# Performance work log

Hardware: AMD Instinct MI355X
Metric: run time of the kernel (lower is better)

The kernel has to match this reference:

```python
import jax, jax.numpy as jnp
import numpy as np

K3 = 27            # kernel_size**3
PAIRS_PER_K = 131072  # pairs per kernel offset (equal-size segments)
N_VOX = 262144     # active voxels (stride-1, same grid: N_in == N_out)
C_IN = 32
C_OUT = 32


def setup_inputs() -> dict:
    key = jax.random.key(0)
    k1, k2, k3, k4 = jax.random.split(key, 4)
    M = K3 * PAIRS_PER_K
    in_feature = jax.random.normal(k1, (N_VOX, C_IN), dtype=jnp.float32)
    kernel = jax.random.normal(k2, (K3, C_IN, C_OUT), dtype=jnp.float32) * (1.0 / np.sqrt(C_IN * K3))
    bias = jax.random.normal(k3, (C_OUT,), dtype=jnp.float32) * 0.01
    # nbmap[:, 0] = input voxel index, nbmap[:, 1] = output voxel index,
    # sorted by kernel offset (offset k owns rows [k*P, (k+1)*P)).
    nbmap = jax.random.randint(k4, (M, 2), 0, N_VOX, dtype=jnp.int32)
    nbsizes = jnp.full((K3,), PAIRS_PER_K, dtype=jnp.int32)
    return {"in_feature": in_feature, "kernel": kernel, "bias": bias,
            "nbmap": nbmap, "nbsizes": nbsizes}


def reference(in_feature, kernel, bias, nbmap, nbsizes):
    """Gather -> per-offset GEMM -> scatter-add, matching
    ext.conv.sparse_convolution for a stride-1 non-transposed conv where
    nbmap rows are grouped by kernel offset with equal segment sizes."""
    k3, c_in, c_out = kernel.shape
    m = nbmap.shape[0]
    p = m // k3  # pairs per offset (static)
    n_out = in_feature.shape[0]  # same grid, stride 1
    # gather input features for every (input, output) pair  [M, C_in]
    gathered = in_feature[nbmap[:, 0]]
    # batched GEMM: one [P, C_in] x [C_in, C_out] per kernel offset
    contrib = jnp.einsum('kpi,kio->kpo', gathered.reshape(k3, p, c_in), kernel)
    contrib = contrib.reshape(m, c_out)
    # scatter-add contributions into output voxels
    out = jax.ops.segment_sum(contrib, nbmap[:, 1], num_segments=n_out)
    return out + bias
```

## Files before the change

### kernel.cpp

```cpp
#include <hip/hip_runtime.h>
#include <hip/hip_bf16.h>


#define N_VOX    262144
#define LOG2_NV  18
#define C_CH     32
#define K3       27
#define LOG2_PPK 17
#define BLOCK    256
#define FLAG_FIN 0x40000000
#define ECAP     4096
#define PLPAD    36
#define FRAGN    (K3 * 2 * 64)
#define NF16     (N_VOX * 4)

typedef __attribute__((ext_vector_type(8))) short bf16x8;
typedef __attribute__((ext_vector_type(4))) float f32x4;

__device__ __forceinline__ unsigned short f2bf(float f) {
  union { __hip_bfloat16 h; unsigned short u; } cv;
  cv.h = __float2bfloat16(f);
  return cv.u;
}

__global__ __launch_bounds__(BLOCK) void setup_kernel(
    int4* __restrict__ clrT, long nt4, int4* __restrict__ clrC, long nc4,
    const float* __restrict__ in_feature, unsigned short* __restrict__ feat16,
    int use16, const float* __restrict__ kernel_w,
    unsigned short* __restrict__ Bf) {
  long idx = (long)blockIdx.x * BLOCK + threadIdx.x;
  if (idx < nt4) {
    clrT[idx] = make_int4(-1, -1, -1, -1);
    return;
  }
  idx -= nt4;
  if (idx < nc4) {
    clrC[idx] = make_int4(0, 0, 0, 0);
    return;
  }
  idx -= nc4;
  if (use16) {
    if (idx < NF16) {
      const float4* src = (const float4*)in_feature + (idx << 1);
      float4 f0 = src[0], f1 = src[1];
      union { unsigned short u[8]; uint4 v; } pk;
      pk.u[0] = f2bf(f0.x); pk.u[1] = f2bf(f0.y);
      pk.u[2] = f2bf(f0.z); pk.u[3] = f2bf(f0.w);
      pk.u[4] = f2bf(f1.x); pk.u[5] = f2bf(f1.y);
      pk.u[6] = f2bf(f1.z); pk.u[7] = f2bf(f1.w);
      ((uint4*)feat16)[idx] = pk.v;
      return;
    }
    idx -= NF16;
  }
  if (idx < FRAGN) {
    int wid = (int)idx;
    int lane = wid & 63;
    int kc = wid >> 6;
    int k = kc >> 1, t = kc & 1;
    int i0 = (lane >> 4) * 8;
    int c = t * 16 + (lane & 15);
    union { unsigned short u[8]; uint4 v; } pk;
#pragma unroll
    for (int j = 0; j < 8; ++j)
      pk.u[j] = f2bf(kernel_w[(k << 10) + (i0 + j) * C_CH + c]);
    ((uint4*)Bf)[wid] = pk.v;
  }
}

__global__ __launch_bounds__(BLOCK) void passA_kernel(
    const int4* __restrict__ nbmap2, int* __restrict__ T, int Mq) {
  int q = blockIdx.x * BLOCK + threadIdx.x;
  if (q >= Mq) return;
  int4 na = nbmap2[q * 2];
  int4 nb = nbmap2[q * 2 + 1];
  int p0 = q << 2, p1 = p0 | 1, p2 = p0 | 2, p3 = p0 | 3;
  T[((p0 >> LOG2_PPK) << LOG2_NV) + na.y] = p0;
  T[((p1 >> LOG2_PPK) << LOG2_NV) + na.w] = p1;
  T[((p2 >> LOG2_PPK) << LOG2_NV) + nb.y] = p2;
  T[((p3 >> LOG2_PPK) << LOG2_NV) + nb.w] = p3;
}

__device__ __forceinline__ void loser_path(
    int vox, int k, int in, int* __restrict__ T2, int idx, int use2,
    int* __restrict__ ovf_cnt, int* __restrict__ ovf, int S2,
    int* __restrict__ ecnt, int2* __restrict__ elist) {
  int val = in;
  if (use2) {
    val = atomicExch(&T2[idx], val);
    if (val < 0) return;
  }
  int pos = atomicAdd(&ovf_cnt[vox], 1);
  if (pos < S2) {
    ovf[(pos << LOG2_NV) + vox] = (k << LOG2_NV) | val;
  } else {
    int ep = atomicAdd(ecnt, 1);
    if (ep < ECAP) elist[ep] = make_int2(vox, (k << LOG2_NV) | val);
  }
}

__global__ __launch_bounds__(BLOCK) void passB_kernel(
    const int4* __restrict__ nbmap2, int* __restrict__ T, int* __restrict__ T2,
    int use2, int* __restrict__ ovf_cnt, int* __restrict__ ovf, int S2,
    int* __restrict__ ecnt, int2* __restrict__ elist, int Mq) {
  int q = blockIdx.x * BLOCK + threadIdx.x;
  if (q >= Mq) return;
  int4 na = nbmap2[q * 2];
  int4 nb = nbmap2[q * 2 + 1];
  int p0 = q << 2, p1 = p0 | 1, p2 = p0 | 2, p3 = p0 | 3;
  int idx0 = ((p0 >> LOG2_PPK) << LOG2_NV) + na.y;
  int idx1 = ((p1 >> LOG2_PPK) << LOG2_NV) + na.w;
  int idx2 = ((p2 >> LOG2_PPK) << LOG2_NV) + nb.y;
  int idx3 = ((p3 >> LOG2_PPK) << LOG2_NV) + nb.w;
  int t0 = T[idx0];
  int t1 = T[idx1];
  int t2 = T[idx2];
  int t3 = T[idx3];
  if (t0 == p0) T[idx0] = FLAG_FIN | na.x;
  else loser_path(na.y, p0 >> LOG2_PPK, na.x, T2, idx0, use2, ovf_cnt, ovf,
                  S2, ecnt, elist);
  if (t1 == p1) T[idx1] = FLAG_FIN | na.z;
  else loser_path(na.w, p1 >> LOG2_PPK, na.z, T2, idx1, use2, ovf_cnt, ovf,
                  S2, ecnt, elist);
  if (t2 == p2) T[idx2] = FLAG_FIN | nb.x;
  else loser_path(nb.y, p2 >> LOG2_PPK, nb.x, T2, idx2, use2, ovf_cnt, ovf,
                  S2, ecnt, elist);
  if (t3 == p3) T[idx3] = FLAG_FIN | nb.z;
  else loser_path(nb.w, p3 >> LOG2_PPK, nb.z, T2, idx3, use2, ovf_cnt, ovf,
                  S2, ecnt, elist);
}

template <int F16>
__global__ __launch_bounds__(BLOCK, 4) void gather_splitk_kernel(
    const float* __restrict__ in_feature,
    const unsigned short* __restrict__ feat16,
    const float* __restrict__ kernel_w,
    const float* __restrict__ bias,
    const int* __restrict__ T,
    const int* __restrict__ T2, int use2,
    const int* __restrict__ ovf_cnt,
    const int* __restrict__ ovf,
    const unsigned short* __restrict__ Bf,
    float* __restrict__ out, int S2) {
  __shared__ float plane[4][16][PLPAD];
  __shared__ int flatE[256];
  __shared__ int scnt[16];

  const int tid = threadIdx.x;
  const int w = tid >> 6;
  const int lane = tid & 63;
  const int r16 = lane & 15;
  const int quad = lane >> 4;
  const int vb = blockIdx.x << 4;

  const int er = tid & 15;
  const int ej = tid >> 4;
  int eval = 0;
  if (ej < S2)
    eval = ovf[(ej << LOG2_NV) + vb + er];
  if (tid < 16) {
    int c = ovf_cnt[vb + tid];
    scnt[tid] = c < S2 ? c : S2;
  }
  const int kb = w * 7;
  const int kn = (w == 3) ? 6 : 7;
  const int v = vb + r16;
  int tv[7];
#pragma unroll
  for (int d = 0; d < 7; ++d)
    tv[d] = (d < kn) ? T[((kb + d) << LOG2_NV) + v] : -1;
  __syncthreads();

  int myb = 0, tot = 0;
#pragma unroll
  for (int q = 0; q < 16; ++q) {
    int cq = scnt[q];
    if (q < er) myb += cq;
    tot += cq;
  }
  if (ej < scnt[er])
    flatE[myb + ej] = (er << 24) | eval;
  __syncthreads();

  int tv2[7];
#pragma unroll
  for (int d = 0; d < 7; ++d)
    tv2[d] = (use2 && d < kn) ? T2[((kb + d) << LOG2_NV) + v] : -1;

  bf16x8 R0[7], R1[7];
#pragma unroll
  for (int d = 0; d < 7; ++d) {
    int t = tv[d];
    int in = (t >= 0) ? (t & 0x3FFFF) : 0;
    bf16x8 a;
    if (F16) {
      a = *reinterpret_cast<const bf16x8*>(feat16 + (in << 5) + (quad << 3));
    } else {
      const float4* ap = (const float4*)(in_feature + (in << 5) + (quad << 3));
      float4 f0 = ap[0], f1 = ap[1];
      a[0] = (short)f2bf(f0.x); a[1] = (short)f2bf(f0.y);
      a[2] = (short)f2bf(f0.z); a[3] = (short)f2bf(f0.w);
      a[4] = (short)f2bf(f1.x); a[5] = (short)f2bf(f1.y);
      a[6] = (short)f2bf(f1.z); a[7] = (short)f2bf(f1.w);
    }
    if (t < 0) a = (bf16x8)0;
    R0[d] = a;
  }
#pragma unroll
  for (int d = 0; d < 7; ++d) {
    int t = tv2[d];
    int in = (t >= 0) ? (t & 0x3FFFF) : 0;
    bf16x8 a;
    if (F16) {
      a = *reinterpret_cast<const bf16x8*>(feat16 + (in << 5) + (quad << 3));
    } else {
      const float4* ap = (const float4*)(in_feature + (in << 5) + (quad << 3));
      float4 f0 = ap[0], f1 = ap[1];
      a[0] = (short)f2bf(f0.x); a[1] = (short)f2bf(f0.y);
      a[2] = (short)f2bf(f0.z); a[3] = (short)f2bf(f0.w);
      a[4] = (short)f2bf(f1.x); a[5] = (short)f2bf(f1.y);
      a[6] = (short)f2bf(f1.z); a[7] = (short)f2bf(f1.w);
    }
    if (t < 0) a = (bf16x8)0;
    R1[d] = a;
  }

  f32x4 acc0 = {0.f, 0.f, 0.f, 0.f};
  f32x4 acc1 = {0.f, 0.f, 0.f, 0.f};
  const uint4* bfp = (const uint4*)Bf;
#pragma unroll
  for (int d = 0; d < 7; ++d) {
    if (d < kn) {
      int k = kb + d;
      uint4 h0 = bfp[(k * 2 + 0) * 64 + lane];
      uint4 h1 = bfp[(k * 2 + 1) * 64 + lane];
      acc0 = __builtin_amdgcn_mfma_f32_16x16x32_bf16(
          R0[d], *reinterpret_cast<const bf16x8*>(&h0), acc0, 0, 0, 0);
      acc1 = __builtin_amdgcn_mfma_f32_16x16x32_bf16(
          R0[d], *reinterpret_cast<const bf16x8*>(&h1), acc1, 0, 0, 0);
    }
  }
  if (use2) {
#pragma unroll
    for (int d = 0; d < 7; ++d) {
      if (d < kn) {
        int k = kb + d;
        uint4 h0 = bfp[(k * 2 + 0) * 64 + lane];
        uint4 h1 = bfp[(k * 2 + 1) * 64 + lane];
        acc0 = __builtin_amdgcn_mfma_f32_16x16x32_bf16(
            R1[d], *reinterpret_cast<const bf16x8*>(&h0), acc0, 0, 0, 0);
        acc1 = __builtin_amdgcn_mfma_f32_16x16x32_bf16(
            R1[d], *reinterpret_cast<const bf16x8*>(&h1), acc1, 0, 0, 0);
      }
    }
  }

#pragma unroll
  for (int reg = 0; reg < 4; ++reg) {
    int row = quad * 4 + reg;
    plane[w][row][r16] = acc0[reg];
    plane[w][row][16 + r16] = acc1[reg];
  }

  const int c32 = lane & 31, h = lane >> 5;
  int i = w;
  int e_cur = 0;
  float4 p0, p1, p2, p3;
  if (i < tot) {
    e_cur = flatE[i];
    const float4* ar =
        (const float4*)(in_feature + ((e_cur & 0x3FFFF) << 5) + (h << 4));
    p0 = ar[0]; p1 = ar[1]; p2 = ar[2]; p3 = ar[3];
  }
  while (i < tot) {
    const int e = e_cur;
    float4 q0 = p0, q1 = p1, q2 = p2, q3 = p3;
    const int inext = i + 4;
    if (inext < tot) {
      e_cur = flatE[inext];
      const float4* ar =
          (const float4*)(in_feature + ((e_cur & 0x3FFFF) << 5) + (h << 4));
      p0 = ar[0]; p1 = ar[1]; p2 = ar[2]; p3 = ar[3];
    }
    const int k2 = (e >> LOG2_NV) & 31;
    const int rr = (e >> 24) & 15;
    const float* wcol = kernel_w + (k2 << 10) + (h << 4) * C_CH + c32;
    float psum = 0.f;
    psum = fmaf(q0.x, wcol[0 * C_CH], psum);
    psum = fmaf(q0.y, wcol[1 * C_CH], psum);
    psum = fmaf(q0.z, wcol[2 * C_CH], psum);
    psum = fmaf(q0.w, wcol[3 * C_CH], psum);
    psum = fmaf(q1.x, wcol[4 * C_CH], psum);
    psum = fmaf(q1.y, wcol[5 * C_CH], psum);
    psum = fmaf(q1.z, wcol[6 * C_CH], psum);
    psum = fmaf(q1.w, wcol[7 * C_CH], psum);
    psum = fmaf(q2.x, wcol[8 * C_CH], psum);
    psum = fmaf(q2.y, wcol[9 * C_CH], psum);
    psum = fmaf(q2.z, wcol[10 * C_CH], psum);
    psum = fmaf(q2.w, wcol[11 * C_CH], psum);
    psum = fmaf(q3.x, wcol[12 * C_CH], psum);
    psum = fmaf(q3.y, wcol[13 * C_CH], psum);
    psum = fmaf(q3.z, wcol[14 * C_CH], psum);
    psum = fmaf(q3.w, wcol[15 * C_CH], psum);
    psum += __shfl_xor(psum, 32);
    if (h == 0) plane[w][rr][c32] += psum;
    i = inext;
  }

  __syncthreads();
  const int mr = tid >> 4;
  const int mc = (tid & 15) << 1;
  float s0 = plane[0][mr][mc] + plane[1][mr][mc] + plane[2][mr][mc] +
             plane[3][mr][mc] + bias[mc];
  float s1 = plane[0][mr][mc + 1] + plane[1][mr][mc + 1] +
             plane[2][mr][mc + 1] + plane[3][mr][mc + 1] + bias[mc + 1];
  float2 o; o.x = s0; o.y = s1;
  *(float2*)(out + ((vb + mr) << 5) + mc) = o;
}

__global__ __launch_bounds__(BLOCK) void emergency_kernel(
    const float* __restrict__ in_feature, const float* __restrict__ kernel_w,
    const int* __restrict__ ecnt, const int2* __restrict__ elist,
    float* __restrict__ out) {
  int e = blockIdx.x * BLOCK + threadIdx.x;
  int n = *ecnt;
  if (n > ECAP) n = ECAP;
  if (e >= n) return;
  int2 ent = elist[e];
  int v = ent.x, k = ent.y >> LOG2_NV, in = ent.y & 0x3FFFF;
  float a[C_CH];
  const float4* ar = (const float4*)(in_feature + (in << 5));
#pragma unroll
  for (int q = 0; q < 8; ++q) ((float4*)a)[q] = ar[q];
  for (int c = 0; c < C_CH; ++c) {
    float s = 0.f;
#pragma unroll
    for (int i = 0; i < C_CH; ++i)
      s = fmaf(a[i], kernel_w[(k << 10) + i * C_CH + c], s);
    atomicAdd(&out[v * C_CH + c], s);
  }
}

__global__ __launch_bounds__(BLOCK) void init_bias_kernel(
    float* __restrict__ out, const float* __restrict__ bias, int n4) {
  int idx = blockIdx.x * blockDim.x + threadIdx.x;
  if (idx >= n4) return;
  ((float4*)out)[idx] = ((const float4*)bias)[idx & 7];
}

__global__ __launch_bounds__(BLOCK) void scatter_conv_kernel(
    const float* __restrict__ in_feature, const float* __restrict__ kernel_w,
    const int* __restrict__ nbmap, float* __restrict__ out) {
  const int k = blockIdx.x >> 9;
  const int pair = blockIdx.x * BLOCK + threadIdx.x;
  const float* __restrict__ Wk = kernel_w + k * (C_CH * C_CH);
  const int2 nb = ((const int2*)nbmap)[pair];
  const float4* __restrict__ inrow =
      (const float4*)(in_feature + (long)nb.x * C_CH);
  float a[C_CH];
#pragma unroll
  for (int j = 0; j < 8; ++j) ((float4*)a)[j] = inrow[j];
  float acc[C_CH];
#pragma unroll
  for (int c = 0; c < C_CH; ++c) acc[c] = 0.0f;
#pragma unroll
  for (int i = 0; i < C_CH; ++i) {
    const float av = a[i];
#pragma unroll
    for (int c = 0; c < C_CH; ++c)
      acc[c] = fmaf(av, Wk[i * C_CH + c], acc[c]);
  }
  float* __restrict__ orow = out + (long)nb.y * C_CH;
#pragma unroll
  for (int c = 0; c < C_CH; ++c) atomicAdd(orow + c, acc[c]);
}

extern "C" void kernel_launch(void* const* d_in, const int* in_sizes, int n_in,
                              void* d_out, int out_size, void* d_ws,
                              size_t ws_size, hipStream_t stream) {
  const float* in_feature = (const float*)d_in[0];
  const float* kernel_w   = (const float*)d_in[1];
  const float* bias       = (const float*)d_in[2];
  const int*   nbmap      = (const int*)d_in[3];
  float* out = (float*)d_out;
  const int M = in_sizes[3] / 2;
  const int Mq = M / 4;

  const long FIXED = 64 + 2 * ECAP + 13824;
  long ws_ints = (long)(ws_size / 4);
  long planes = (ws_ints - FIXED) / N_VOX;
  int use2 = 0, use16 = 0;
  long s2c;
  if (planes >= 75) {
    use2 = 1; use16 = 1;
    s2c = planes - 71;
    if (s2c > 7) s2c = 7;
  } else if (planes >= 59) {
    use2 = 1;
    s2c = planes - 55;
    if (s2c > 7) s2c = 7;
  } else {
    s2c = planes - 28;
    if (s2c > 15) s2c = 15;
  }
  int S2 = (int)s2c;

  if (!use2 && S2 < 4) {
    const int n4 = out_size / 4;
    init_bias_kernel<<<(n4 + BLOCK - 1) / BLOCK, BLOCK, 0, stream>>>(out, bias,
                                                                     n4);
    scatter_conv_kernel<<<M / BLOCK, BLOCK, 0, stream>>>(in_feature, kernel_w,
                                                         nbmap, out);
    return;
  }

  const long TPLANES = (long)K3 * N_VOX;
  int* T        = (int*)d_ws;
  int* T2       = use2 ? (T + TPLANES) : T;
  int* ovf_cnt  = T + TPLANES * (1 + use2);
  int* ecnt     = ovf_cnt + N_VOX;
  int2* elist   = (int2*)(ecnt + 64);
  unsigned short* Bf = (unsigned short*)(ecnt + 64 + 2 * ECAP);
  int* ovf      = ((int*)Bf) + 13824;
  unsigned short* feat16 = (unsigned short*)(ovf + (long)S2 * N_VOX);

  const long nt4 = TPLANES * (1 + use2) / 4;
  const long nc4 = (N_VOX + 64) / 4;
  const long total = nt4 + nc4 + (use16 ? (long)NF16 : 0) + FRAGN;
  const long sblocks = (total + BLOCK - 1) / BLOCK;
  setup_kernel<<<(int)sblocks, BLOCK, 0, stream>>>(
      (int4*)T, nt4, (int4*)ovf_cnt, nc4, in_feature, feat16, use16, kernel_w,
      Bf);

  passA_kernel<<<(Mq + BLOCK - 1) / BLOCK, BLOCK, 0, stream>>>(
      (const int4*)nbmap, T, Mq);
  passB_kernel<<<(Mq + BLOCK - 1) / BLOCK, BLOCK, 0, stream>>>(
      (const int4*)nbmap, T, T2, use2, ovf_cnt, ovf, S2, ecnt, elist, Mq);
  if (use16)
    gather_splitk_kernel<1><<<N_VOX / 16, BLOCK, 0, stream>>>(
        in_feature, feat16, kernel_w, bias, T, T2, use2, ovf_cnt, ovf, Bf,
        out, S2);
  else
    gather_splitk_kernel<0><<<N_VOX / 16, BLOCK, 0, stream>>>(
        in_feature, feat16, kernel_w, bias, T, T2, use2, ovf_cnt, ovf, Bf,
        out, S2);
  emergency_kernel<<<ECAP / BLOCK, BLOCK, 0, stream>>>(in_feature, kernel_w,
                                                       ecnt, elist, out);
}
```

Measured before the change: 393.9 us.

## Pack primary and secondary slot into one 64-bit table entry per (offset, voxel)

Replaces the two separate 32-bit tables T and T2 with a single 64-bit table whose entries hold the winning pair id, its input index, and a second input index. Pass A writes pair id and input together, so pass B no longer needs to write winners back, and losers claim the second slot with a 64-bit CAS instead of an atomicExch on a separate plane. The gather kernel then reads one 8-byte word per offset instead of two scattered 4-byte reads. The aim is fewer random memory transactions in passes B and gather, at the cost of CAS retry loops and wider stores in pass A.

```diff
diff --git a/kernel.cpp b/kernel.cpp
--- a/kernel.cpp
+++ b/kernel.cpp
@@ -16,6 +16,10 @@
 
 typedef __attribute__((ext_vector_type(8))) short bf16x8;
 typedef __attribute__((ext_vector_type(4))) float f32x4;
+typedef unsigned long long ull;
+
+#define PMASK   0x3FFFFFull
+#define EMPTY2(w) (((w) >> 58) == 0x3Full)
 
 __device__ __forceinline__ unsigned short f2bf(float f) {
   union { __hip_bfloat16 h; unsigned short u; } cv;
@@ -68,76 +72,105 @@
   }
 }
 
-__global__ __launch_bounds__(BLOCK) void passA_kernel(
-    const int4* __restrict__ nbmap2, int* __restrict__ T, int Mq) {
+__global__ __launch_bounds__(BLOCK) void passA_packed(
+    const int4* __restrict__ nbmap2, ull* __restrict__ T64, int Mq) {
   int q = blockIdx.x * BLOCK + threadIdx.x;
   if (q >= Mq) return;
   int4 na = nbmap2[q * 2];
   int4 nb = nbmap2[q * 2 + 1];
   int p0 = q << 2, p1 = p0 | 1, p2 = p0 | 2, p3 = p0 | 3;
-  T[((p0 >> LOG2_PPK) << LOG2_NV) + na.y] = p0;
-  T[((p1 >> LOG2_PPK) << LOG2_NV) + na.w] = p1;
-  T[((p2 >> LOG2_PPK) << LOG2_NV) + nb.y] = p2;
-  T[((p3 >> LOG2_PPK) << LOG2_NV) + nb.w] = p3;
-}
-
-__device__ __forceinline__ void loser_path(
-    int vox, int k, int in, int* __restrict__ T2, int idx, int use2,
+  const ull EM = 0x3Full << 58;
+  T64[((long)(p0 >> LOG2_PPK) << LOG2_NV) + na.y] =
+      (ull)p0 | ((ull)na.x << 22) | EM;
+  T64[((long)(p1 >> LOG2_PPK) << LOG2_NV) + na.w] =
+      (ull)p1 | ((ull)na.z << 22) | EM;
+  T64[((long)(p2 >> LOG2_PPK) << LOG2_NV) + nb.y] =
+      (ull)p2 | ((ull)nb.x << 22) | EM;
+  T64[((long)(p3 >> LOG2_PPK) << LOG2_NV) + nb.w] =
+      (ull)p3 | ((ull)nb.z << 22) | EM;
+}
+
+__device__ __forceinline__ void ovf_push(
+    int vox, int k, int in, int* __restrict__ ovf_cnt, int* __restrict__ ovf,
+    int S2, int* __restrict__ ecnt, int2* __restrict__ elist) {
+  int pos = atomicAdd(&ovf_cnt[vox], 1);
+  if (pos < S2) {
+    ovf[(pos << LOG2_NV) + vox] = (k << LOG2_NV) | in;
+  } else {
+    int ep = atomicAdd(ecnt, 1);
+    if (ep < ECAP) elist[ep] = make_int2(vox, (k << LOG2_NV) | in);
+  }
+}
+
+__device__ __forceinline__ void resolve_packed(
+    int p, int vox, int in, ull w, ull* __restrict__ T64, long idx,
     int* __restrict__ ovf_cnt, int* __restrict__ ovf, int S2,
     int* __restrict__ ecnt, int2* __restrict__ elist) {
-  int val = in;
-  if (use2) {
-    val = atomicExch(&T2[idx], val);
-    if (val < 0) return;
-  }
-  int pos = atomicAdd(&ovf_cnt[vox], 1);
-  if (pos < S2) {
-    ovf[(pos << LOG2_NV) + vox] = (k << LOG2_NV) | val;
-  } else {
-    int ep = atomicAdd(ecnt, 1);
-    if (ep < ECAP) elist[ep] = make_int2(vox, (k << LOG2_NV) | val);
-  }
-}
-
-__global__ __launch_bounds__(BLOCK) void passB_kernel(
-    const int4* __restrict__ nbmap2, int* __restrict__ T, int* __restrict__ T2,
-    int use2, int* __restrict__ ovf_cnt, int* __restrict__ ovf, int S2,
+  if ((w & PMASK) == (ull)p) return;
+  ull cur = w;
+  for (;;) {
+    if (!EMPTY2(cur)) break;
+    ull nw = (cur & ((1ull << 40) - 1)) | ((ull)in << 40);
+    ull old = atomicCAS(&T64[idx], cur, nw);
+    if (old == cur) return;
+    cur = old;
+  }
+  ovf_push(vox, p >> LOG2_PPK, in, ovf_cnt, ovf, S2, ecnt, elist);
+}
+
+__global__ __launch_bounds__(BLOCK) void passB_packed(
+    const int4* __restrict__ nbmap2, ull* __restrict__ T64,
+    int* __restrict__ ovf_cnt, int* __restrict__ ovf, int S2,
     int* __restrict__ ecnt, int2* __restrict__ elist, int Mq) {
   int q = blockIdx.x * BLOCK + threadIdx.x;
   if (q >= Mq) return;
   int4 na = nbmap2[q * 2];
   int4 nb = nbmap2[q * 2 + 1];
   int p0 = q << 2, p1 = p0 | 1, p2 = p0 | 2, p3 = p0 | 3;
-  int idx0 = ((p0 >> LOG2_PPK) << LOG2_NV) + na.y;
-  int idx1 = ((p1 >> LOG2_PPK) << LOG2_NV) + na.w;
-  int idx2 = ((p2 >> LOG2_PPK) << LOG2_NV) + nb.y;
-  int idx3 = ((p3 >> LOG2_PPK) << LOG2_NV) + nb.w;
-  int t0 = T[idx0];
-  int t1 = T[idx1];
-  int t2 = T[idx2];
-  int t3 = T[idx3];
-  if (t0 == p0) T[idx0] = FLAG_FIN | na.x;
-  else loser_path(na.y, p0 >> LOG2_PPK, na.x, T2, idx0, use2, ovf_cnt, ovf,
-                  S2, ecnt, elist);
-  if (t1 == p1) T[idx1] = FLAG_FIN | na.z;
-  else loser_path(na.w, p1 >> LOG2_PPK, na.z, T2, idx1, use2, ovf_cnt, ovf,
-                  S2, ecnt, elist);
-  if (t2 == p2) T[idx2] = FLAG_FIN | nb.x;
-  else loser_path(nb.y, p2 >> LOG2_PPK, nb.x, T2, idx2, use2, ovf_cnt, ovf,
-                  S2, ecnt, elist);
-  if (t3 == p3) T[idx3] = FLAG_FIN | nb.z;
-  else loser_path(nb.w, p3 >> LOG2_PPK, nb.z, T2, idx3, use2, ovf_cnt, ovf,
-                  S2, ecnt, elist);
-}
-
-template <int F16>
+  long i0 = ((long)(p0 >> LOG2_PPK) << LOG2_NV) + na.y;
+  long i1 = ((long)(p1 >> LOG2_PPK) << LOG2_NV) + na.w;
+  long i2 = ((long)(p2 >> LOG2_PPK) << LOG2_NV) + nb.y;
+  long i3 = ((long)(p3 >> LOG2_PPK) << LOG2_NV) + nb.w;
+  ull w0 = T64[i0];
+  ull w1 = T64[i1];
+  ull w2 = T64[i2];
+  ull w3 = T64[i3];
+  resolve_packed(p0, na.y, na.x, w0, T64, i0, ovf_cnt, ovf, S2, ecnt, elist);
+  resolve_packed(p1, na.w, na.z, w1, T64, i1, ovf_cnt, ovf, S2, ecnt, elist);
+  resolve_packed(p2, nb.y, nb.x, w2, T64, i2, ovf_cnt, ovf, S2, ecnt, elist);
+  resolve_packed(p3, nb.w, nb.z, w3, T64, i3, ovf_cnt, ovf, S2, ecnt, elist);
+}
+
+__global__ __launch_bounds__(BLOCK) void passA_legacy(
+    const int2* __restrict__ nbmap, int* __restrict__ T, int M) {
+  int p = blockIdx.x * BLOCK + threadIdx.x;
+  if (p >= M) return;
+  int2 nb = nbmap[p];
+  T[((p >> LOG2_PPK) << LOG2_NV) + nb.y] = p;
+}
+
+__global__ __launch_bounds__(BLOCK) void passB_legacy(
+    const int2* __restrict__ nbmap, int* __restrict__ T,
+    int* __restrict__ ovf_cnt, int* __restrict__ ovf, int S2,
+    int* __restrict__ ecnt, int2* __restrict__ elist, int M) {
+  int p = blockIdx.x * BLOCK + threadIdx.x;
+  if (p >= M) return;
+  int2 nb = nbmap[p];
+  int idx = ((p >> LOG2_PPK) << LOG2_NV) + nb.y;
+  if (T[idx] == p) {
+    T[idx] = FLAG_FIN | nb.x;
+  } else {
+    ovf_push(nb.y, p >> LOG2_PPK, nb.x, ovf_cnt, ovf, S2, ecnt, elist);
+  }
+}
+
+template <int PACKED, int F16>
 __global__ __launch_bounds__(BLOCK, 4) void gather_splitk_kernel(
     const float* __restrict__ in_feature,
     const unsigned short* __restrict__ feat16,
     const float* __restrict__ kernel_w,
     const float* __restrict__ bias,
-    const int* __restrict__ T,
-    const int* __restrict__ T2, int use2,
+    const void* __restrict__ Tv,
     const int* __restrict__ ovf_cnt,
     const int* __restrict__ ovf,
     const unsigned short* __restrict__ Bf,
@@ -165,10 +198,22 @@
   const int kb = w * 7;
   const int kn = (w == 3) ? 6 : 7;
   const int v = vb + r16;
-  int tv[7];
-#pragma unroll
-  for (int d = 0; d < 7; ++d)
-    tv[d] = (d < kn) ? T[((kb + d) << LOG2_NV) + v] : -1;
+
+  ull wv[7];
+  if (PACKED) {
+    const ull* T64 = (const ull*)Tv;
+#pragma unroll
+    for (int d = 0; d < 7; ++d)
+      wv[d] = (d < kn) ? T64[((long)(kb + d) << LOG2_NV) + v] : ~0ull;
+  } else {
+    const int* T = (const int*)Tv;
+#pragma unroll
+    for (int d = 0; d < 7; ++d) {
+      int t = (d < kn) ? T[((kb + d) << LOG2_NV) + v] : -1;
+      wv[d] = (t >= 0) ? (((ull)(t & 0x3FFFF) << 22) | (0x3Full << 58))
+                       : ~0ull;
+    }
+  }
   __syncthreads();
 
   int myb = 0, tot = 0;
@@ -182,16 +227,11 @@
     flatE[myb + ej] = (er << 24) | eval;
   __syncthreads();
 
-  int tv2[7];
-#pragma unroll
-  for (int d = 0; d < 7; ++d)
-    tv2[d] = (use2 && d < kn) ? T2[((kb + d) << LOG2_NV) + v] : -1;
-
   bf16x8 R0[7], R1[7];
 #pragma unroll
   for (int d = 0; d < 7; ++d) {
-    int t = tv[d];
-    int in = (t >= 0) ? (t & 0x3FFFF) : 0;
+    bool val1 = (wv[d] & PMASK) != PMASK;
+    int in = val1 ? (int)((wv[d] >> 22) & 0x3FFFF) : 0;
     bf16x8 a;
     if (F16) {
       a = *reinterpret_cast<const bf16x8*>(feat16 + (in << 5) + (quad << 3));
@@ -203,26 +243,29 @@
       a[4] = (short)f2bf(f1.x); a[5] = (short)f2bf(f1.y);
       a[6] = (short)f2bf(f1.z); a[7] = (short)f2bf(f1.w);
     }
-    if (t < 0) a = (bf16x8)0;
+    if (!val1) a = (bf16x8)0;
     R0[d] = a;
   }
-#pragma unroll
-  for (int d = 0; d < 7; ++d) {
-    int t = tv2[d];
-    int in = (t >= 0) ? (t & 0x3FFFF) : 0;
-    bf16x8 a;
-    if (F16) {
-      a = *reinterpret_cast<const bf16x8*>(feat16 + (in << 5) + (quad << 3));
-    } else {
-      const float4* ap = (const float4*)(in_feature + (in << 5) + (quad << 3));
-      float4 f0 = ap[0], f1 = ap[1];
-      a[0] = (short)f2bf(f0.x); a[1] = (short)f2bf(f0.y);
-      a[2] = (short)f2bf(f0.z); a[3] = (short)f2bf(f0.w);
-      a[4] = (short)f2bf(f1.x); a[5] = (short)f2bf(f1.y);
-      a[6] = (short)f2bf(f1.z); a[7] = (short)f2bf(f1.w);
-    }
-    if (t < 0) a = (bf16x8)0;
-    R1[d] = a;
+  if (PACKED) {
+#pragma unroll
+    for (int d = 0; d < 7; ++d) {
+      bool val2 = !EMPTY2(wv[d]);
+      int in = val2 ? (int)((wv[d] >> 40) & 0x3FFFF) : 0;
+      bf16x8 a;
+      if (F16) {
+        a = *reinterpret_cast<const bf16x8*>(feat16 + (in << 5) + (quad << 3));
+      } else {
+        const float4* ap =
+            (const float4*)(in_feature + (in << 5) + (quad << 3));
+        float4 f0 = ap[0], f1 = ap[1];
+        a[0] = (short)f2bf(f0.x); a[1] = (short)f2bf(f0.y);
+        a[2] = (short)f2bf(f0.z); a[3] = (short)f2bf(f0.w);
+        a[4] = (short)f2bf(f1.x); a[5] = (short)f2bf(f1.y);
+        a[6] = (short)f2bf(f1.z); a[7] = (short)f2bf(f1.w);
+      }
+      if (!val2) a = (bf16x8)0;
+      R1[d] = a;
+    }
   }
 
   f32x4 acc0 = {0.f, 0.f, 0.f, 0.f};
@@ -240,7 +283,7 @@
           R0[d], *reinterpret_cast<const bf16x8*>(&h1), acc1, 0, 0, 0);
     }
   }
-  if (use2) {
+  if (PACKED) {
 #pragma unroll
     for (int d = 0; d < 7; ++d) {
       if (d < kn) {
@@ -389,14 +432,14 @@
   const long FIXED = 64 + 2 * ECAP + 13824;
   long ws_ints = (long)(ws_size / 4);
   long planes = (ws_ints - FIXED) / N_VOX;
-  int use2 = 0, use16 = 0;
+  int packed = 0, use16 = 0;
   long s2c;
   if (planes >= 75) {
-    use2 = 1; use16 = 1;
+    packed = 1; use16 = 1;
     s2c = planes - 71;
     if (s2c > 7) s2c = 7;
   } else if (planes >= 59) {
-    use2 = 1;
+    packed = 1;
     s2c = planes - 55;
     if (s2c > 7) s2c = 7;
   } else {
@@ -405,7 +448,7 @@
   }
   int S2 = (int)s2c;
 
-  if (!use2 && S2 < 4) {
+  if (!packed && S2 < 4) {
     const int n4 = out_size / 4;
     init_bias_kernel<<<(n4 + BLOCK - 1) / BLOCK, BLOCK, 0, stream>>>(out, bias,
                                                                      n4);
@@ -414,36 +457,45 @@
     return;
   }
 
-  const long TPLANES = (long)K3 * N_VOX;
-  int* T        = (int*)d_ws;
-  int* T2       = use2 ? (T + TPLANES) : T;
-  int* ovf_cnt  = T + TPLANES * (1 + use2);
+  const long planesT = packed ? 2L * K3 : (long)K3;
+  int* Tbase    = (int*)d_ws;
+  int* ovf_cnt  = Tbase + planesT * N_VOX;
   int* ecnt     = ovf_cnt + N_VOX;
   int2* elist   = (int2*)(ecnt + 64);
   unsigned short* Bf = (unsigned short*)(ecnt + 64 + 2 * ECAP);
   int* ovf      = ((int*)Bf) + 13824;
   unsigned short* feat16 = (unsigned short*)(ovf + (long)S2 * N_VOX);
 
-  const long nt4 = TPLANES * (1 + use2) / 4;
+  const long nt4 = planesT * N_VOX / 4;
   const long nc4 = (N_VOX + 64) / 4;
   const long total = nt4 + nc4 + (use16 ? (long)NF16 : 0) + FRAGN;
   const long sblocks = (total + BLOCK - 1) / BLOCK;
   setup_kernel<<<(int)sblocks, BLOCK, 0, stream>>>(
-      (int4*)T, nt4, (int4*)ovf_cnt, nc4, in_feature, feat16, use16, kernel_w,
-      Bf);
-
-  passA_kernel<<<(Mq + BLOCK - 1) / BLOCK, BLOCK, 0, stream>>>(
-      (const int4*)nbmap, T, Mq);
-  passB_kernel<<<(Mq + BLOCK - 1) / BLOCK, BLOCK, 0, stream>>>(
-      (const int4*)nbmap, T, T2, use2, ovf_cnt, ovf, S2, ecnt, elist, Mq);
-  if (use16)
-    gather_splitk_kernel<1><<<N_VOX / 16, BLOCK, 0, stream>>>(
-        in_feature, feat16, kernel_w, bias, T, T2, use2, ovf_cnt, ovf, Bf,
-        out, S2);
-  else
-    gather_splitk_kernel<0><<<N_VOX / 16, BLOCK, 0, stream>>>(
-        in_feature, feat16, kernel_w, bias, T, T2, use2, ovf_cnt, ovf, Bf,
-        out, S2);
+      (int4*)Tbase, nt4, (int4*)ovf_cnt, nc4, in_feature, feat16, use16,
+      kernel_w, Bf);
+
+  if (packed) {
+    passA_packed<<<(Mq + BLOCK - 1) / BLOCK, BLOCK, 0, stream>>>(
+        (const int4*)nbmap, (ull*)Tbase, Mq);
+    passB_packed<<<(Mq + BLOCK - 1) / BLOCK, BLOCK, 0, stream>>>(
+        (const int4*)nbmap, (ull*)Tbase, ovf_cnt, ovf, S2, ecnt, elist, Mq);
+    if (use16)
+      gather_splitk_kernel<1, 1><<<N_VOX / 16, BLOCK, 0, stream>>>(
+          in_feature, feat16, kernel_w, bias, (const void*)Tbase, ovf_cnt,
+          ovf, Bf, out, S2);
+    else
+      gather_splitk_kernel<1, 0><<<N_VOX / 16, BLOCK, 0, stream>>>(
+          in_feature, feat16, kernel_w, bias, (const void*)Tbase, ovf_cnt,
+          ovf, Bf, out, S2);
+  } else {
+    passA_legacy<<<(M + BLOCK - 1) / BLOCK, BLOCK, 0, stream>>>(
+        (const int2*)nbmap, Tbase, M);
+    passB_legacy<<<(M + BLOCK - 1) / BLOCK, BLOCK, 0, stream>>>(
+        (const int2*)nbmap, Tbase, ovf_cnt, ovf, S2, ecnt, elist, M);
+    gather_splitk_kernel<0, 0><<<N_VOX / 16, BLOCK, 0, stream>>>(
+        in_feature, feat16, kernel_w, bias, (const void*)Tbase, ovf_cnt, ovf,
+        Bf, out, S2);
+  }
   emergency_kernel<<<ECAP / BLOCK, BLOCK, 0, stream>>>(in_feature, kernel_w,
                                                        ecnt, elist, out);
 }
```

After: 362.0 us, median of 3. -8.1%, faster.

## Replace dense per-offset tables with sliced bucketed pair lists for gather

Applied to the files above, without the earlier changes.

Drops the two dense K3×N_VOX lookup planes and the two-pass claim/overflow scheme. A single scatter pass appends each pair into per-16-voxel buckets, split into 8 slices to spread atomic contention. The gather kernel now builds the per-offset slots in shared memory from those buckets, and the emergency list is folded into the gather kernel, so the separate fallback kernel launch is gone. This removes clearing and reading ~56 MB of tables, at the cost of global atomics on bucket counters, LDS atomics, and every block scanning the global overflow list.

```diff
diff --git a/kernel.cpp b/kernel.cpp
--- a/kernel.cpp
+++ b/kernel.cpp
@@ -8,11 +8,13 @@
 #define K3       27
 #define LOG2_PPK 17
 #define BLOCK    256
-#define FLAG_FIN 0x40000000
 #define ECAP     4096
 #define PLPAD    36
 #define FRAGN    (K3 * 2 * 64)
 #define NF16     (N_VOX * 4)
+#define NBUCK    16384
+#define SCAP     64
+#define NSLOT    (K3 * 16)
 
 typedef __attribute__((ext_vector_type(8))) short bf16x8;
 typedef __attribute__((ext_vector_type(4))) float f32x4;
@@ -24,16 +26,11 @@
 }
 
 __global__ __launch_bounds__(BLOCK) void setup_kernel(
-    int4* __restrict__ clrT, long nt4, int4* __restrict__ clrC, long nc4,
+    int4* __restrict__ clrC, long nc4,
     const float* __restrict__ in_feature, unsigned short* __restrict__ feat16,
     int use16, const float* __restrict__ kernel_w,
     unsigned short* __restrict__ Bf) {
   long idx = (long)blockIdx.x * BLOCK + threadIdx.x;
-  if (idx < nt4) {
-    clrT[idx] = make_int4(-1, -1, -1, -1);
-    return;
-  }
-  idx -= nt4;
   if (idx < nc4) {
     clrC[idx] = make_int4(0, 0, 0, 0);
     return;
@@ -68,130 +65,112 @@
   }
 }
 
-__global__ __launch_bounds__(BLOCK) void passA_kernel(
-    const int4* __restrict__ nbmap2, int* __restrict__ T, int Mq) {
+__device__ __forceinline__ void put_pair(
+    int vox, int in, int k, int slice, int* __restrict__ cnt,
+    int* __restrict__ bucket, int* __restrict__ ecnt,
+    int2* __restrict__ elist) {
+  int sb = slice * NBUCK + (vox >> 4);
+  int pos = atomicAdd(&cnt[sb], 1);
+  if (pos < SCAP) {
+    bucket[(long)sb * SCAP + pos] = (k << 22) | ((vox & 15) << 18) | in;
+  } else {
+    int ep = atomicAdd(ecnt, 1);
+    if (ep < ECAP) elist[ep] = make_int2(vox, (k << LOG2_NV) | in);
+  }
+}
+
+__global__ __launch_bounds__(BLOCK) void scatter_pairs(
+    const int4* __restrict__ nbmap2, int* __restrict__ cnt,
+    int* __restrict__ bucket, int* __restrict__ ecnt,
+    int2* __restrict__ elist, int Mq) {
   int q = blockIdx.x * BLOCK + threadIdx.x;
   if (q >= Mq) return;
+  int slice = blockIdx.x & 7;
   int4 na = nbmap2[q * 2];
   int4 nb = nbmap2[q * 2 + 1];
-  int p0 = q << 2, p1 = p0 | 1, p2 = p0 | 2, p3 = p0 | 3;
-  T[((p0 >> LOG2_PPK) << LOG2_NV) + na.y] = p0;
-  T[((p1 >> LOG2_PPK) << LOG2_NV) + na.w] = p1;
-  T[((p2 >> LOG2_PPK) << LOG2_NV) + nb.y] = p2;
-  T[((p3 >> LOG2_PPK) << LOG2_NV) + nb.w] = p3;
-}
-
-__device__ __forceinline__ void loser_path(
-    int vox, int k, int in, int* __restrict__ T2, int idx, int use2,
-    int* __restrict__ ovf_cnt, int* __restrict__ ovf, int S2,
-    int* __restrict__ ecnt, int2* __restrict__ elist) {
-  int val = in;
-  if (use2) {
-    val = atomicExch(&T2[idx], val);
-    if (val < 0) return;
-  }
-  int pos = atomicAdd(&ovf_cnt[vox], 1);
-  if (pos < S2) {
-    ovf[(pos << LOG2_NV) + vox] = (k << LOG2_NV) | val;
-  } else {
-    int ep = atomicAdd(ecnt, 1);
-    if (ep < ECAP) elist[ep] = make_int2(vox, (k << LOG2_NV) | val);
-  }
-}
-
-__global__ __launch_bounds__(BLOCK) void passB_kernel(
-    const int4* __restrict__ nbmap2, int* __restrict__ T, int* __restrict__ T2,
-    int use2, int* __restrict__ ovf_cnt, int* __restrict__ ovf, int S2,
-    int* __restrict__ ecnt, int2* __restrict__ elist, int Mq) {
-  int q = blockIdx.x * BLOCK + threadIdx.x;
-  if (q >= Mq) return;
-  int4 na = nbmap2[q * 2];
-  int4 nb = nbmap2[q * 2 + 1];
-  int p0 = q << 2, p1 = p0 | 1, p2 = p0 | 2, p3 = p0 | 3;
-  int idx0 = ((p0 >> LOG2_PPK) << LOG2_NV) + na.y;
-  int idx1 = ((p1 >> LOG2_PPK) << LOG2_NV) + na.w;
-  int idx2 = ((p2 >> LOG2_PPK) << LOG2_NV) + nb.y;
-  int idx3 = ((p3 >> LOG2_PPK) << LOG2_NV) + nb.w;
-  int t0 = T[idx0];
-  int t1 = T[idx1];
-  int t2 = T[idx2];
-  int t3 = T[idx3];
-  if (t0 == p0) T[idx0] = FLAG_FIN | na.x;
-  else loser_path(na.y, p0 >> LOG2_PPK, na.x, T2, idx0, use2, ovf_cnt, ovf,
-                  S2, ecnt, elist);
-  if (t1 == p1) T[idx1] = FLAG_FIN | na.z;
-  else loser_path(na.w, p1 >> LOG2_PPK, na.z, T2, idx1, use2, ovf_cnt, ovf,
-                  S2, ecnt, elist);
-  if (t2 == p2) T[idx2] = FLAG_FIN | nb.x;
-  else loser_path(nb.y, p2 >> LOG2_PPK, nb.x, T2, idx2, use2, ovf_cnt, ovf,
-                  S2, ecnt, elist);
-  if (t3 == p3) T[idx3] = FLAG_FIN | nb.z;
-  else loser_path(nb.w, p3 >> LOG2_PPK, nb.z, T2, idx3, use2, ovf_cnt, ovf,
-                  S2, ecnt, elist);
+  int p0 = q << 2;
+  put_pair(na.y, na.x, (p0 | 0) >> LOG2_PPK, slice, cnt, bucket, ecnt, elist);
+  put_pair(na.w, na.z, (p0 | 1) >> LOG2_PPK, slice, cnt, bucket, ecnt, elist);
+  put_pair(nb.y, nb.x, (p0 | 2) >> LOG2_PPK, slice, cnt, bucket, ecnt, elist);
+  put_pair(nb.w, nb.z, (p0 | 3) >> LOG2_PPK, slice, cnt, bucket, ecnt, elist);
 }
 
 template <int F16>
-__global__ __launch_bounds__(BLOCK, 4) void gather_splitk_kernel(
+__global__ __launch_bounds__(BLOCK, 4) void gather_csr_kernel(
     const float* __restrict__ in_feature,
     const unsigned short* __restrict__ feat16,
     const float* __restrict__ kernel_w,
     const float* __restrict__ bias,
-    const int* __restrict__ T,
-    const int* __restrict__ T2, int use2,
-    const int* __restrict__ ovf_cnt,
-    const int* __restrict__ ovf,
+    const int* __restrict__ cnt,
+    const int* __restrict__ bucket,
+    const int* __restrict__ ecnt,
+    const int2* __restrict__ elist,
     const unsigned short* __restrict__ Bf,
-    float* __restrict__ out, int S2) {
+    float* __restrict__ out) {
   __shared__ float plane[4][16][PLPAD];
-  __shared__ int flatE[256];
-  __shared__ int scnt[16];
+  __shared__ int flatE[320];
+  __shared__ int ls1[NSLOT], ls2[NSLOT];
+  __shared__ int lcnt[NSLOT];
+  __shared__ int scn[8];
+  __shared__ int extraN;
 
   const int tid = threadIdx.x;
   const int w = tid >> 6;
   const int lane = tid & 63;
   const int r16 = lane & 15;
   const int quad = lane >> 4;
-  const int vb = blockIdx.x << 4;
-
-  const int er = tid & 15;
-  const int ej = tid >> 4;
-  int eval = 0;
-  if (ej < S2)
-    eval = ovf[(ej << LOG2_NV) + vb + er];
-  if (tid < 16) {
-    int c = ovf_cnt[vb + tid];
-    scnt[tid] = c < S2 ? c : S2;
-  }
+  const int b = blockIdx.x;
+  const int vb = b << 4;
+
+  for (int i = tid; i < NSLOT; i += BLOCK) {
+    ls1[i] = -1; ls2[i] = -1; lcnt[i] = 0;
+  }
+  if (tid < 8) scn[tid] = min(cnt[tid * NBUCK + b], SCAP);
+  if (tid == 0) extraN = 0;
+  __syncthreads();
+
+  {
+    const int s = tid >> 5;
+    const int i0 = tid & 31;
+    const int n = scn[s];
+    const int* base = bucket + (long)(s * NBUCK + b) * SCAP;
+    for (int i = i0; i < n; i += 32) {
+      int e = base[i];
+      int sl = (e >> 18) & 511;
+      int in = e & 0x3FFFF;
+      int pos = atomicAdd(&lcnt[sl], 1);
+      if (pos == 0) ls1[sl] = in;
+      else if (pos == 1) ls2[sl] = in;
+      else {
+        int x = atomicAdd(&extraN, 1);
+        if (x < 320)
+          flatE[x] = (((e >> 18) & 15) << 24) | (((e >> 22) & 31) << 18) | in;
+      }
+    }
+  }
+  if (tid < 64) {
+    int ne = *ecnt;
+    if (ne > ECAP) ne = ECAP;
+    for (int e2 = tid; e2 < ne; e2 += 64) {
+      int2 ent = elist[e2];
+      unsigned dv = (unsigned)(ent.x - vb);
+      if (dv < 16u) {
+        int x = atomicAdd(&extraN, 1);
+        if (x < 320) flatE[x] = (dv << 24) | ent.y;
+      }
+    }
+  }
+  __syncthreads();
+  int tot = extraN;
+  if (tot > 320) tot = 320;
+
   const int kb = w * 7;
   const int kn = (w == 3) ? 6 : 7;
-  const int v = vb + r16;
-  int tv[7];
-#pragma unroll
-  for (int d = 0; d < 7; ++d)
-    tv[d] = (d < kn) ? T[((kb + d) << LOG2_NV) + v] : -1;
-  __syncthreads();
-
-  int myb = 0, tot = 0;
-#pragma unroll
-  for (int q = 0; q < 16; ++q) {
-    int cq = scnt[q];
-    if (q < er) myb += cq;
-    tot += cq;
-  }
-  if (ej < scnt[er])
-    flatE[myb + ej] = (er << 24) | eval;
-  __syncthreads();
-
-  int tv2[7];
-#pragma unroll
-  for (int d = 0; d < 7; ++d)
-    tv2[d] = (use2 && d < kn) ? T2[((kb + d) << LOG2_NV) + v] : -1;
-
   bf16x8 R0[7], R1[7];
 #pragma unroll
   for (int d = 0; d < 7; ++d) {
-    int t = tv[d];
-    int in = (t >= 0) ? (t & 0x3FFFF) : 0;
+    int t = (d < kn) ? ls1[(kb + d) * 16 + r16] : -1;
+    int in = (t >= 0) ? t : 0;
     bf16x8 a;
     if (F16) {
       a = *reinterpret_cast<const bf16x8*>(feat16 + (in << 5) + (quad << 3));
@@ -208,8 +187,8 @@
   }
 #pragma unroll
   for (int d = 0; d < 7; ++d) {
-    int t = tv2[d];
-    int in = (t >= 0) ? (t & 0x3FFFF) : 0;
+    int t = (d < kn) ? ls2[(kb + d) * 16 + r16] : -1;
+    int in = (t >= 0) ? t : 0;
     bf16x8 a;
     if (F16) {
       a = *reinterpret_cast<const bf16x8*>(feat16 + (in << 5) + (quad << 3));
@@ -240,18 +219,16 @@
           R0[d], *reinterpret_cast<const bf16x8*>(&h1), acc1, 0, 0, 0);
     }
   }
-  if (use2) {
-#pragma unroll
-    for (int d = 0; d < 7; ++d) {
-      if (d < kn) {
-        int k = kb + d;
-        uint4 h0 = bfp[(k * 2 + 0) * 64 + lane];
-        uint4 h1 = bfp[(k * 2 + 1) * 64 + lane];
-        acc0 = __builtin_amdgcn_mfma_f32_16x16x32_bf16(
-            R1[d], *reinterpret_cast<const bf16x8*>(&h0), acc0, 0, 0, 0);
-        acc1 = __builtin_amdgcn_mfma_f32_16x16x32_bf16(
-            R1[d], *reinterpret_cast<const bf16x8*>(&h1), acc1, 0, 0, 0);
-      }
+#pragma unroll
+  for (int d = 0; d < 7; ++d) {
+    if (d < kn) {
+      int k = kb + d;
+      uint4 h0 = bfp[(k * 2 + 0) * 64 + lane];
+      uint4 h1 = bfp[(k * 2 + 1) * 64 + lane];
+      acc0 = __builtin_amdgcn_mfma_f32_16x16x32_bf16(
+          R1[d], *reinterpret_cast<const bf16x8*>(&h0), acc0, 0, 0, 0);
+      acc1 = __builtin_amdgcn_mfma_f32_16x16x32_bf16(
+          R1[d], *reinterpret_cast<const bf16x8*>(&h1), acc1, 0, 0, 0);
     }
   }
 
@@ -318,29 +295,6 @@
   *(float2*)(out + ((vb + mr) << 5) + mc) = o;
 }
 
-__global__ __launch_bounds__(BLOCK) void emergency_kernel(
-    const float* __restrict__ in_feature, const float* __restrict__ kernel_w,
-    const int* __restrict__ ecnt, const int2* __restrict__ elist,
-    float* __restrict__ out) {
-  int e = blockIdx.x * BLOCK + threadIdx.x;
-  int n = *ecnt;
-  if (n > ECAP) n = ECAP;
-  if (e >= n) return;
-  int2 ent = elist[e];
-  int v = ent.x, k = ent.y >> LOG2_NV, in = ent.y & 0x3FFFF;
-  float a[C_CH];
-  const float4* ar = (const float4*)(in_feature + (in << 5));
-#pragma unroll
-  for (int q = 0; q < 8; ++q) ((float4*)a)[q] = ar[q];
-  for (int c = 0; c < C_CH; ++c) {
-    float s = 0.f;
-#pragma unroll
-    for (int i = 0; i < C_CH; ++i)
-      s = fmaf(a[i], kernel_w[(k << 10) + i * C_CH + c], s);
-    atomicAdd(&out[v * C_CH + c], s);
-  }
-}
-
 __global__ __launch_bounds__(BLOCK) void init_bias_kernel(
     float* __restrict__ out, const float* __restrict__ bias, int n4) {
   int idx = blockIdx.x * blockDim.x + threadIdx.x;
@@ -386,26 +340,16 @@
   const int M = in_sizes[3] / 2;
   const int Mq = M / 4;
 
-  const long FIXED = 64 + 2 * ECAP + 13824;
+  const long CNT_I   = 8L * NBUCK;
+  const long HDR_I   = CNT_I + 64 + 2 * ECAP + 13824;
+  const long BUCK_I  = 8L * NBUCK * SCAP;
+  const long F16_I   = (long)N_VOX * 16;
   long ws_ints = (long)(ws_size / 4);
-  long planes = (ws_ints - FIXED) / N_VOX;
-  int use2 = 0, use16 = 0;
-  long s2c;
-  if (planes >= 75) {
-    use2 = 1; use16 = 1;
-    s2c = planes - 71;
-    if (s2c > 7) s2c = 7;
-  } else if (planes >= 59) {
-    use2 = 1;
-    s2c = planes - 55;
-    if (s2c > 7) s2c = 7;
-  } else {
-    s2c = planes - 28;
-    if (s2c > 15) s2c = 15;
-  }
-  int S2 = (int)s2c;
-
-  if (!use2 && S2 < 4) {
+  int use16 = 0, csr = 0;
+  if (ws_ints >= HDR_I + BUCK_I + F16_I) { csr = 1; use16 = 1; }
+  else if (ws_ints >= HDR_I + BUCK_I)    { csr = 1; }
+
+  if (!csr) {
     const int n4 = out_size / 4;
     init_bias_kernel<<<(n4 + BLOCK - 1) / BLOCK, BLOCK, 0, stream>>>(out, bias,
                                                                      n4);
@@ -414,36 +358,26 @@
     return;
   }
 
-  const long TPLANES = (long)K3 * N_VOX;
-  int* T        = (int*)d_ws;
-  int* T2       = use2 ? (T + TPLANES) : T;
-  int* ovf_cnt  = T + TPLANES * (1 + use2);
-  int* ecnt     = ovf_cnt + N_VOX;
+  int* cnt      = (int*)d_ws;
+  int* ecnt     = cnt + CNT_I;
   int2* elist   = (int2*)(ecnt + 64);
   unsigned short* Bf = (unsigned short*)(ecnt + 64 + 2 * ECAP);
-  int* ovf      = ((int*)Bf) + 13824;
-  unsigned short* feat16 = (unsigned short*)(ovf + (long)S2 * N_VOX);
-
-  const long nt4 = TPLANES * (1 + use2) / 4;
-  const long nc4 = (N_VOX + 64) / 4;
-  const long total = nt4 + nc4 + (use16 ? (long)NF16 : 0) + FRAGN;
+  int* bucket   = ((int*)Bf) + 13824;
+  unsigned short* feat16 = (unsigned short*)(bucket + BUCK_I);
+
+  const long nc4 = (CNT_I + 64) / 4;
+  const long total = nc4 + (use16 ? (long)NF16 : 0) + FRAGN;
   const long sblocks = (total + BLOCK - 1) / BLOCK;
   setup_kernel<<<(int)sblocks, BLOCK, 0, stream>>>(
-      (int4*)T, nt4, (int4*)ovf_cnt, nc4, in_feature, feat16, use16, kernel_w,
-      Bf);
-
-  passA_kernel<<<(Mq + BLOCK - 1) / BLOCK, BLOCK, 0, stream>>>(
-      (const int4*)nbmap, T, Mq);
-  passB_kernel<<<(Mq + BLOCK - 1) / BLOCK, BLOCK, 0, stream>>>(
-      (const int4*)nbmap, T, T2, use2, ovf_cnt, ovf, S2, ecnt, elist, Mq);
+      (int4*)cnt, nc4, in_feature, feat16, use16, kernel_w, Bf);
+
+  scatter_pairs<<<(Mq + BLOCK - 1) / BLOCK, BLOCK, 0, stream>>>(
+      (const int4*)nbmap, cnt, bucket, ecnt, elist, Mq);
+
   if (use16)
-    gather_splitk_kernel<1><<<N_VOX / 16, BLOCK, 0, stream>>>(
-        in_feature, feat16, kernel_w, bias, T, T2, use2, ovf_cnt, ovf, Bf,
-        out, S2);
+    gather_csr_kernel<1><<<NBUCK, BLOCK, 0, stream>>>(
+        in_feature, feat16, kernel_w, bias, cnt, bucket, ecnt, elist, Bf, out);
   else
-    gather_splitk_kernel<0><<<N_VOX / 16, BLOCK, 0, stream>>>(
-        in_feature, feat16, kernel_w, bias, T, T2, use2, ovf_cnt, ovf, Bf,
-        out, S2);
-  emergency_kernel<<<ECAP / BLOCK, BLOCK, 0, stream>>>(in_feature, kernel_w,
-                                                       ecnt, elist, out);
-}
+    gather_csr_kernel<0><<<NBUCK, BLOCK, 0, stream>>>(
+        in_feature, feat16, kernel_w, bias, cnt, bucket, ecnt, elist, Bf, out);
+}
```

Result: faster. 375.6 us (-4.7%).
